# Optimization experiments

Hardware: AMD Instinct MI355X
Metric: run time of the kernel (lower is better)

Reference implementation:

```python
import jax, jax.numpy as jnp
import numpy as np

GRID_SIZE = 128
FEATURE_SIZE = 16
HIDDEN_SIZE = 64
N_POINTS = 2097152


def setup_inputs() -> dict:
    key = jax.random.key(0)
    ks = jax.random.split(key, 8)
    points = jax.random.uniform(ks[0], (N_POINTS, 3), dtype=jnp.float32)
    grid = jax.random.normal(ks[1], (GRID_SIZE, GRID_SIZE, GRID_SIZE, FEATURE_SIZE), dtype=jnp.float32)
    # torch nn.Linear default init: U(-1/sqrt(fan_in), 1/sqrt(fan_in))
    def linear(k, fan_in, fan_out):
        kw, kb = jax.random.split(k)
        bound = 1.0 / np.sqrt(fan_in)
        W = jax.random.uniform(kw, (fan_out, fan_in), minval=-bound, maxval=bound, dtype=jnp.float32)
        b = jax.random.uniform(kb, (fan_out,), minval=-bound, maxval=bound, dtype=jnp.float32)
        return W, b
    W1, b1 = linear(ks[2], FEATURE_SIZE, HIDDEN_SIZE)
    W2, b2 = linear(ks[3], HIDDEN_SIZE, HIDDEN_SIZE)
    W3, b3 = linear(ks[4], HIDDEN_SIZE, 1)
    return {"points": points, "grid": grid, "W1": W1, "b1": b1,
            "W2": W2, "b2": b2, "W3": W3, "b3": b3}


def reference(points, grid, W1, b1, W2, b2, W3, b3):
    gs = grid.shape[0]
    # nearest-grid-node index: scale to [0, gs-1], clamp, round
    p = jnp.clip(points * (gs - 1), 0.0, gs - 1)
    idx = jnp.round(p).astype(jnp.int32)  # (N, 3)
    feats = grid[idx[:, 0], idx[:, 1], idx[:, 2]]  # (N, F) gather
    h = jax.nn.relu(feats @ W1.T + b1)
    h = jax.nn.relu(h @ W2.T + b2)
    occ = jnp.tanh(h @ W3.T + b3)  # (N, 1)
    return occ
```

## Files before the change

kernel.cpp:

```cpp
#include <hip/hip_runtime.h>
#include <hip/hip_fp16.h>
#include <cstdint>
#include <cstddef>


typedef _Float16 half8 __attribute__((ext_vector_type(8)));
typedef __fp16  fp16v2 __attribute__((ext_vector_type(2)));
typedef float float4v __attribute__((ext_vector_type(4)));

#define WPB 4
#define NT  16
#define NP  8
#define FD  5

__device__ inline uint32_t relu_pk(float a, float b) {
    union { fp16v2 h; uint32_t u; } c;
    fp16v2 h = __builtin_amdgcn_cvt_pkrtz(a, b);
    fp16v2 z = {};
    c.h = __builtin_elementwise_max(h, z);
    return c.u;
}

__global__ __launch_bounds__(256, 3) void occ_mlp_kernel(
    const float* __restrict__ pts,
    const float* __restrict__ grid,
    const float* __restrict__ W1, const float* __restrict__ b1,
    const float* __restrict__ W2, const float* __restrict__ b2,
    const float* __restrict__ W3, const float* __restrict__ b3,
    float* __restrict__ out, int nPoints)
{
    const int lane = threadIdx.x & 63;
    const int l15  = lane & 15;
    const int quad = lane >> 4;
    const int wib  = threadIdx.x >> 6;
    const int tile0 = (blockIdx.x * WPB + wib) * NT;
    const int nTiles = (nPoints + 15) >> 4;
    if (tile0 >= nTiles) return;
    const int maxP = nPoints - 1;
    const int pt0  = tile0 << 4;

    const int half = quad & 1;
    const int tsel = quad >> 1;

    half8 A1[4];
#pragma unroll
    for (int t = 0; t < 4; ++t) {
        half8 f = {};
        if (quad < 2) {
            const float* row = W1 + (16 * t + l15) * 16 + quad * 8;
#pragma unroll
            for (int j = 0; j < 8; ++j) f[j] = (_Float16)row[j];
        } else if (quad == 2) {
            f[0] = (_Float16)b1[16 * t + l15];
        }
        A1[t] = f;
    }
    half8 A2[4][2];
#pragma unroll
    for (int t = 0; t < 4; ++t)
#pragma unroll
        for (int kk = 0; kk < 2; ++kk) {
            const float* row = W2 + (16 * t + l15) * 64 + 32 * kk + 8 * quad;
            half8 f;
#pragma unroll
            for (int j = 0; j < 8; ++j) f[j] = (_Float16)row[j];
            A2[t][kk] = f;
        }
    float4v bias2[4];
    float w3v[4][4];
#pragma unroll
    for (int t = 0; t < 4; ++t)
#pragma unroll
        for (int r = 0; r < 4; ++r) {
            int h = 16 * t + 4 * quad + r;
            bias2[t][r] = b2[h];
            w3v[t][r]   = W3[h];
        }
    const float bias3 = b3[0];

    const int src0 = l15 + 16 * ((2 * quad) & 3);
    const int src1 = l15 + 16 * ((2 * quad + 1) & 3);
    const bool sel = (quad >> 1) != 0;

    float Cx[3], Cy[3], Cz[3];
    float4 Fa[FD], Fb[FD];

    auto loadCoords = [&](int slot, int v) {
        int p = pt0 + v * 32 + (tsel << 4) + l15;
        p = p > maxP ? maxP : p;
        const float* q = pts + 3 * p;
        Cx[slot] = q[0]; Cy[slot] = q[1]; Cz[slot] = q[2];
    };
    auto loadFeat = [&](int fslot, int cslot) {
        const int ix = (int)rintf(fminf(fmaxf(Cx[cslot] * 127.0f, 0.0f), 127.0f));
        const int iy = (int)rintf(fminf(fmaxf(Cy[cslot] * 127.0f, 0.0f), 127.0f));
        const int iz = (int)rintf(fminf(fmaxf(Cz[cslot] * 127.0f, 0.0f), 127.0f));
        const int ofs = ((((ix << 7) | iy) << 7) | iz) << 4;
        const float4* g = reinterpret_cast<const float4*>(grid + ofs + (half << 3));
        Fa[fslot] = g[0];
        Fb[fslot] = g[1];
    };

    loadCoords(0, 0); loadCoords(1, 1); loadCoords(2, 2);
    loadFeat(0, 0); loadFeat(1, 1); loadFeat(2, 2);
    loadCoords(0, 3); loadCoords(1, 4);
    loadFeat(3, 0); loadFeat(4, 1);
    loadCoords(2, 5); loadCoords(0, 6);

    float o[4];

#pragma unroll
    for (int v = 0; v < NP; ++v) {
        const int s = v % FD;

        const float4 a0 = Fa[s];
        const float4 a1 = Fb[s];
        float4 b0, b1v;
        b0.x  = __shfl_xor(Fa[s].x, 32); b0.y  = __shfl_xor(Fa[s].y, 32);
        b0.z  = __shfl_xor(Fa[s].z, 32); b0.w  = __shfl_xor(Fa[s].w, 32);
        b1v.x = __shfl_xor(Fb[s].x, 32); b1v.y = __shfl_xor(Fb[s].y, 32);
        b1v.z = __shfl_xor(Fb[s].z, 32); b1v.w = __shfl_xor(Fb[s].w, 32);

        if (v + FD < NP) loadFeat(s, (v + FD) % 3);
        if (v + 7  < NP) loadCoords((v + 7) % 3, v + 7);

#pragma unroll
        for (int tt = 0; tt < 2; ++tt) {
            const int u = 2 * v + tt;
            const float4 f0 = tt ? b0 : a0;
            const float4 f1 = tt ? b1v : a1;

            half8 bfrag = {};
            if (quad < 2) {
                bfrag[0] = (_Float16)f0.x; bfrag[1] = (_Float16)f0.y;
                bfrag[2] = (_Float16)f0.z; bfrag[3] = (_Float16)f0.w;
                bfrag[4] = (_Float16)f1.x; bfrag[5] = (_Float16)f1.y;
                bfrag[6] = (_Float16)f1.z; bfrag[7] = (_Float16)f1.w;
            } else if (quad == 2) {
                bfrag[0] = (_Float16)1.0f;
            }

            float4v C1[4];
#pragma unroll
            for (int t = 0; t < 4; ++t) {
                float4v zacc = {};
                C1[t] = __builtin_amdgcn_mfma_f32_16x16x32_f16(A1[t], bfrag, zacc, 0, 0, 0);
            }

            uint32_t P[4][2];
#pragma unroll
            for (int t = 0; t < 4; ++t) {
                P[t][0] = relu_pk(C1[t][0], C1[t][1]);
                P[t][1] = relu_pk(C1[t][2], C1[t][3]);
            }

            union Frag { uint32_t u[4]; half8 h; } B2[2];
#pragma unroll
            for (int kk = 0; kk < 2; ++kk) {
                const uint32_t x0a = (uint32_t)__shfl((int)P[2 * kk    ][0], src0);
                const uint32_t x0b = (uint32_t)__shfl((int)P[2 * kk + 1][0], src0);
                const uint32_t x1a = (uint32_t)__shfl((int)P[2 * kk    ][1], src0);
                const uint32_t x1b = (uint32_t)__shfl((int)P[2 * kk + 1][1], src0);
                const uint32_t y0a = (uint32_t)__shfl((int)P[2 * kk    ][0], src1);
                const uint32_t y0b = (uint32_t)__shfl((int)P[2 * kk + 1][0], src1);
                const uint32_t y1a = (uint32_t)__shfl((int)P[2 * kk    ][1], src1);
                const uint32_t y1b = (uint32_t)__shfl((int)P[2 * kk + 1][1], src1);
                B2[kk].u[0] = sel ? x0b : x0a;
                B2[kk].u[1] = sel ? x1b : x1a;
                B2[kk].u[2] = sel ? y0b : y0a;
                B2[kk].u[3] = sel ? y1b : y1a;
            }

            float4v C2[4];
#pragma unroll
            for (int t = 0; t < 4; ++t) C2[t] = bias2[t];
#pragma unroll
            for (int kk = 0; kk < 2; ++kk)
#pragma unroll
                for (int t = 0; t < 4; ++t)
                    C2[t] = __builtin_amdgcn_mfma_f32_16x16x32_f16(A2[t][kk], B2[kk].h, C2[t], 0, 0, 0);

            float z = 0.0f;
#pragma unroll
            for (int t = 0; t < 4; ++t)
#pragma unroll
                for (int r = 0; r < 4; ++r)
                    z = fmaf(fmaxf(C2[t][r], 0.0f), w3v[t][r], z);
            z += __shfl_xor(z, 16);
            z += __shfl_xor(z, 32);
            const float e = __expf(2.0f * (z + bias3));
            o[u & 3] = fmaf(-2.0f, __builtin_amdgcn_rcpf(e + 1.0f), 1.0f);

            if ((u & 3) == 3) {
                const float osel = (quad == 0) ? o[0] : (quad == 1) ? o[1]
                                 : (quad == 2) ? o[2] : o[3];
                const int pstore = (tile0 + (u & ~3)) * 16 + lane;
                if (pstore <= maxP) out[pstore] = osel;
            }
        }

        asm volatile("" ::: "memory");
    }
}

extern "C" void kernel_launch(void* const* d_in, const int* in_sizes, int n_in,
                              void* d_out, int out_size, void* d_ws, size_t ws_size,
                              hipStream_t stream)
{
    const float* pts  = (const float*)d_in[0];
    const float* grid = (const float*)d_in[1];
    const float* W1   = (const float*)d_in[2];
    const float* b1   = (const float*)d_in[3];
    const float* W2   = (const float*)d_in[4];
    const float* b2   = (const float*)d_in[5];
    const float* W3   = (const float*)d_in[6];
    const float* b3   = (const float*)d_in[7];
    float* out = (float*)d_out;
    const int nPoints = in_sizes[0] / 3;

    const int nTiles = (nPoints + 15) >> 4;
    const int tilesPerBlock = WPB * NT;
    const int nBlocks = (nTiles + tilesPerBlock - 1) / tilesPerBlock;

    occ_mlp_kernel<<<dim3(nBlocks), dim3(256), 0, stream>>>(
        pts, grid, W1, b1, W2, b2, W3, b3, out, nPoints);
}
```

Before: 274.4 us.

## Stage MLP weight fragments in LDS and shorten gather prefetch depth

```diff
diff --git a/kernel.cpp b/kernel.cpp
--- a/kernel.cpp
+++ b/kernel.cpp
@@ -11,7 +11,6 @@
 #define WPB 4
 #define NT  16
 #define NP  8
-#define FD  5
 
 __device__ inline uint32_t relu_pk(float a, float b) {
     union { fp16v2 h; uint32_t u; } c;
@@ -29,22 +28,19 @@
     const float* __restrict__ W3, const float* __restrict__ b3,
     float* __restrict__ out, int nPoints)
 {
+    __shared__ half8 wlds[768];
+
     const int lane = threadIdx.x & 63;
     const int l15  = lane & 15;
     const int quad = lane >> 4;
     const int wib  = threadIdx.x >> 6;
     const int tile0 = (blockIdx.x * WPB + wib) * NT;
     const int nTiles = (nPoints + 15) >> 4;
-    if (tile0 >= nTiles) return;
     const int maxP = nPoints - 1;
     const int pt0  = tile0 << 4;
 
-    const int half = quad & 1;
-    const int tsel = quad >> 1;
-
-    half8 A1[4];
-#pragma unroll
-    for (int t = 0; t < 4; ++t) {
+    {
+        const int t = wib;
         half8 f = {};
         if (quad < 2) {
             const float* row = W1 + (16 * t + l15) * 16 + quad * 8;
@@ -53,19 +49,22 @@
         } else if (quad == 2) {
             f[0] = (_Float16)b1[16 * t + l15];
         }
-        A1[t] = f;
-    }
-    half8 A2[4][2];
-#pragma unroll
-    for (int t = 0; t < 4; ++t)
+        wlds[t * 64 + lane] = f;
 #pragma unroll
         for (int kk = 0; kk < 2; ++kk) {
             const float* row = W2 + (16 * t + l15) * 64 + 32 * kk + 8 * quad;
-            half8 f;
-#pragma unroll
-            for (int j = 0; j < 8; ++j) f[j] = (_Float16)row[j];
-            A2[t][kk] = f;
-        }
+            half8 g;
+#pragma unroll
+            for (int j = 0; j < 8; ++j) g[j] = (_Float16)row[j];
+            wlds[256 + (t * 2 + kk) * 64 + lane] = g;
+        }
+    }
+    __syncthreads();
+    if (tile0 >= nTiles) return;
+
+    const int half = quad & 1;
+    const int tsel = quad >> 1;
+
     float4v bias2[4];
     float w3v[4][4];
 #pragma unroll
@@ -83,7 +82,7 @@
     const bool sel = (quad >> 1) != 0;
 
     float Cx[3], Cy[3], Cz[3];
-    float4 Fa[FD], Fb[FD];
+    float4 Fa[4], Fb[4];
 
     auto loadCoords = [&](int slot, int v) {
         int p = pt0 + v * 32 + (tsel << 4) + l15;
@@ -104,14 +103,12 @@
     loadCoords(0, 0); loadCoords(1, 1); loadCoords(2, 2);
     loadFeat(0, 0); loadFeat(1, 1); loadFeat(2, 2);
     loadCoords(0, 3); loadCoords(1, 4);
-    loadFeat(3, 0); loadFeat(4, 1);
-    loadCoords(2, 5); loadCoords(0, 6);
 
     float o[4];
 
 #pragma unroll
     for (int v = 0; v < NP; ++v) {
-        const int s = v % FD;
+        const int s = v & 3;
 
         const float4 a0 = Fa[s];
         const float4 a1 = Fb[s];
@@ -121,8 +118,8 @@
         b1v.x = __shfl_xor(Fb[s].x, 32); b1v.y = __shfl_xor(Fb[s].y, 32);
         b1v.z = __shfl_xor(Fb[s].z, 32); b1v.w = __shfl_xor(Fb[s].w, 32);
 
-        if (v + FD < NP) loadFeat(s, (v + FD) % 3);
-        if (v + 7  < NP) loadCoords((v + 7) % 3, v + 7);
+        if (v + 3 < NP) loadFeat((v + 3) & 3, v % 3);
+        if (v + 5 < NP) loadCoords((v + 2) % 3, v + 5);
 
 #pragma unroll
         for (int tt = 0; tt < 2; ++tt) {
@@ -140,18 +137,14 @@
                 bfrag[0] = (_Float16)1.0f;
             }
 
-            float4v C1[4];
+            uint32_t P[4][2];
 #pragma unroll
             for (int t = 0; t < 4; ++t) {
+                const half8 a1f = wlds[t * 64 + lane];
                 float4v zacc = {};
-                C1[t] = __builtin_amdgcn_mfma_f32_16x16x32_f16(A1[t], bfrag, zacc, 0, 0, 0);
-            }
-
-            uint32_t P[4][2];
-#pragma unroll
-            for (int t = 0; t < 4; ++t) {
-                P[t][0] = relu_pk(C1[t][0], C1[t][1]);
-                P[t][1] = relu_pk(C1[t][2], C1[t][3]);
+                const float4v C1 = __builtin_amdgcn_mfma_f32_16x16x32_f16(a1f, bfrag, zacc, 0, 0, 0);
+                P[t][0] = relu_pk(C1[0], C1[1]);
+                P[t][1] = relu_pk(C1[2], C1[3]);
             }
 
             union Frag { uint32_t u[4]; half8 h; } B2[2];
@@ -177,8 +170,10 @@
 #pragma unroll
             for (int kk = 0; kk < 2; ++kk)
 #pragma unroll
-                for (int t = 0; t < 4; ++t)
-                    C2[t] = __builtin_amdgcn_mfma_f32_16x16x32_f16(A2[t][kk], B2[kk].h, C2[t], 0, 0, 0);
+                for (int t = 0; t < 4; ++t) {
+                    const half8 a2f = wlds[256 + (t * 2 + kk) * 64 + lane];
+                    C2[t] = __builtin_amdgcn_mfma_f32_16x16x32_f16(a2f, B2[kk].h, C2[t], 0, 0, 0);
+                }
 
             float z = 0.0f;
 #pragma unroll
```

Measured after the change: 239.5 us. 12.7% less time.
